# Performance work log

Hardware: AMD Instinct MI355X
Metric: run time of the kernel (lower is better)

Reference implementation:

```python
import jax, jax.numpy as jnp
import numpy as np

N = 10000      # cells (nodes)
F_IN = 512     # genes (features)
H = 40         # hidden_dim
DEG = 16       # avg kNN degree
EPS = 1e-5     # GraphNorm eps


def gcn(x, W, b, src, dst, coef):
    # PyG GCNConv: transform then symmetric-normalized aggregate (+bias)
    h = x @ W                                   # [N, out]
    msg = h[src] * coef[:, None]                # [E, out]
    out = jax.ops.segment_sum(msg, dst, num_segments=N)
    return out + b


def graph_norm(x, weight, bias, alpha):
    # PyG GraphNorm over a single graph: mean/var across nodes, learnable mean scale
    mean = jnp.mean(x, axis=0, keepdims=True)
    shifted = x - alpha * mean
    var = jnp.mean(shifted * shifted, axis=0, keepdims=True)
    return weight * shifted * jax.lax.rsqrt(var + EPS) + bias


def setup_inputs() -> dict:
    key = jax.random.key(0)
    ks = jax.random.split(key, 8)
    x = jax.random.uniform(ks[0], (N, F_IN), dtype=jnp.float32)
    E = N * DEG
    src = jax.random.randint(ks[1], (E,), 0, N)
    dst = jax.random.randint(ks[2], (E,), 0, N)
    loop = jnp.arange(N)
    src = jnp.concatenate([src, loop])          # add self-loops (GCNConv default)
    dst = jnp.concatenate([dst, loop])

    def glorot(k, shape):
        lim = np.sqrt(6.0 / (shape[0] + shape[1])).astype(np.float32)
        return jax.random.uniform(k, shape, jnp.float32, -lim, lim)

    W1 = glorot(ks[3], (F_IN, H)); b1 = jnp.zeros((H,), jnp.float32)
    gn_w = jnp.ones((H,), jnp.float32)
    gn_b = jnp.zeros((H,), jnp.float32)
    gn_a = jnp.ones((H,), jnp.float32)          # mean_scale alpha
    Wm = glorot(ks[4], (H, F_IN)); bm = jnp.zeros((F_IN,), jnp.float32)
    Wd = glorot(ks[5], (H, F_IN)); bd = jnp.zeros((F_IN,), jnp.float32)
    Wp = glorot(ks[6], (H, F_IN)); bp = jnp.zeros((F_IN,), jnp.float32)
    return {"x": x, "src": src, "dst": dst, "W1": W1, "b1": b1,
            "gn_w": gn_w, "gn_b": gn_b, "gn_a": gn_a,
            "Wm": Wm, "bm": bm, "Wd": Wd, "bd": bd, "Wp": Wp, "bp": bp}


def reference(x, src, dst, W1, b1, gn_w, gn_b, gn_a, Wm, bm, Wd, bd, Wp, bp):
    # symmetric GCN normalization (self-loops already in edge list, so deg >= 1)
    deg = jax.ops.segment_sum(jnp.ones_like(src, dtype=x.dtype), dst, num_segments=N)
    dis = jax.lax.rsqrt(deg)
    coef = dis[src] * dis[dst]                  # [E]

    hidden = jax.nn.relu(graph_norm(gcn(x, W1, b1, src, dst, coef), gn_w, gn_b, gn_a))
    # Dropout(0.3) is identity at inference
    _mean = jnp.clip(jnp.exp(gcn(hidden, Wm, bm, src, dst, coef)), 1e-5, 1e6)
    _disp = jnp.clip(jax.nn.softplus(gcn(hidden, Wd, bd, src, dst, coef)), 1e-4, 1e4)
    _pi = jax.nn.sigmoid(gcn(hidden, Wp, bp, src, dst, coef))
    return (_mean, _disp, _pi)
```

## Files before the change

### kernel.cpp

```cpp
#include <hip/hip_runtime.h>
#include <math.h>

#define NN 10000
#define FIN 512
#define HD 40
#define GEPS 1e-5f

#define ZI4 ((2 * NN + 2 * HD) / 4)
#define MM1_BLOCKS ((NN + 15) / 16)
#define ZERO_BLOCKS ((ZI4 + 255) / 256)

typedef _Float16 h4 __attribute__((ext_vector_type(4)));
typedef float f4 __attribute__((ext_vector_type(4)));

__global__ void k_hist(const int* __restrict__ dst, int* __restrict__ cnt, int E) {
    int e = blockIdx.x * blockDim.x + threadIdx.x;
    if (e < E) atomicAdd(&cnt[dst[e]], 1);
}

__global__ __launch_bounds__(1024) void k_scan(const int* __restrict__ cnt,
                                               int* __restrict__ rowstart,
                                               float* __restrict__ dis) {
    __shared__ int lds[1024];
    const int t = threadIdx.x;
    const int start = t * 10;
    const int end = min(start + 10, NN);
    int s = 0;
    for (int i = start; i < end; ++i) s += cnt[i];
    lds[t] = s;
    __syncthreads();
    for (int off = 1; off < 1024; off <<= 1) {
        int v = (t >= off) ? lds[t - off] : 0;
        __syncthreads();
        lds[t] += v;
        __syncthreads();
    }
    int run = lds[t] - s;
    for (int i = start; i < end; ++i) {
        int c = cnt[i];
        rowstart[i] = run;
        run += c;
        dis[i] = rsqrtf((float)c);
    }
    if (end == NN) rowstart[NN] = run;
}

__global__ void k_fill(const int* __restrict__ src, const int* __restrict__ dst,
                       const int* __restrict__ rowstart, int* __restrict__ cur,
                       const float* __restrict__ dis, int2* __restrict__ csr, int E) {
    int e = blockIdx.x * blockDim.x + threadIdx.x;
    if (e >= E) return;
    int s = src[e], d = dst[e];
    int pos = rowstart[d] + atomicAdd(&cur[d], 1);
    int2 v;
    v.x = s;
    v.y = __float_as_int(dis[s] * dis[d]);
    csr[pos] = v;
}

__global__ void k_cvtW(const float* __restrict__ Wm, const float* __restrict__ Wd,
                       const float* __restrict__ Wp, _Float16* __restrict__ Whf) {
    int idx = blockIdx.x * 256 + threadIdx.x;
    if (idx >= 3 * 32 * 3 * 64) return;
    int lane = idx & 63;
    int kk   = (idx >> 6) % 3;
    int ct   = ((idx >> 6) / 3) % 32;
    int z    = idx / (64 * 3 * 32);
    const float* W = (z == 0) ? Wm : (z == 1) ? Wd : Wp;
    int col = ct * 16 + (lane & 15);
    h4 v;
#pragma unroll
    for (int j = 0; j < 4; ++j) {
        int krow = kk * 16 + (lane >> 4) * 4 + j;
        v[j] = (krow < HD) ? (_Float16)W[(size_t)krow * FIN + col] : (_Float16)0.f;
    }
    *(h4*)(Whf + (size_t)idx * 4) = v;
}

__global__ __launch_bounds__(256) void k_mm1z(const float* __restrict__ x,
                                              const float* __restrict__ W1,
                                              float* __restrict__ h1,
                                              int4* __restrict__ zbuf) {
    if (blockIdx.x >= MM1_BLOCKS) {
        int i = (blockIdx.x - MM1_BLOCKS) * 256 + threadIdx.x;
        if (i < ZI4) zbuf[i] = make_int4(0, 0, 0, 0);
        return;
    }
    __shared__ float red[256 * 41];
    const int tid = threadIdx.x;
    const int r = tid & 15;
    const int kg = tid >> 4;
    const int row = blockIdx.x * 16 + r;
    const int rowc = min(row, NN - 1);
    const float4* xr = (const float4*)(x + (size_t)rowc * FIN + kg * 32);
    float acc[HD];
#pragma unroll
    for (int c = 0; c < HD; ++c) acc[c] = 0.f;
#pragma unroll 2
    for (int q = 0; q < 8; ++q) {
        float4 xv = xr[q];
        const float* wbase = W1 + (size_t)(kg * 32 + q * 4) * HD;
#pragma unroll
        for (int kk = 0; kk < 4; ++kk) {
            float xs = (kk == 0) ? xv.x : (kk == 1) ? xv.y : (kk == 2) ? xv.z : xv.w;
#pragma unroll
            for (int c4 = 0; c4 < 10; ++c4) {
                float4 wv = *(const float4*)(wbase + kk * HD + c4 * 4);
                acc[c4 * 4 + 0] = fmaf(xs, wv.x, acc[c4 * 4 + 0]);
                acc[c4 * 4 + 1] = fmaf(xs, wv.y, acc[c4 * 4 + 1]);
                acc[c4 * 4 + 2] = fmaf(xs, wv.z, acc[c4 * 4 + 2]);
                acc[c4 * 4 + 3] = fmaf(xs, wv.w, acc[c4 * 4 + 3]);
            }
        }
    }
#pragma unroll
    for (int c = 0; c < HD; ++c) red[tid * 41 + c] = acc[c];
    __syncthreads();
    if (tid < 160) {
        int rr = tid / 10, c4 = tid % 10;
        float o0 = 0.f, o1 = 0.f, o2 = 0.f, o3 = 0.f;
#pragma unroll
        for (int kg2 = 0; kg2 < 16; ++kg2) {
            const float* p = &red[(kg2 * 16 + rr) * 41 + c4 * 4];
            o0 += p[0]; o1 += p[1]; o2 += p[2]; o3 += p[3];
        }
        int orow = blockIdx.x * 16 + rr;
        if (orow < NN)
            *(float4*)&h1[(size_t)orow * HD + c4 * 4] = make_float4(o0, o1, o2, o3);
    }
}

template <bool NORM>
__global__ __launch_bounds__(256) void k_gather(const int* __restrict__ rowstart,
                                                const int2* __restrict__ csr,
                                                const float* __restrict__ hin,
                                                const float* __restrict__ stats,
                                                const float* __restrict__ b1,
                                                const float* __restrict__ gw,
                                                const float* __restrict__ gb,
                                                const float* __restrict__ ga,
                                                float* __restrict__ aggout_f,
                                                _Float16* __restrict__ aggout_h) {
    __shared__ float4 part[256];
    __shared__ float csc[2 * HD];
    const int t = threadIdx.x;
    if (NORM) {
        if (t < HD) {
            float m   = stats[t] * (1.0f / NN);
            float ex2 = stats[HD + t] * (1.0f / NN);
            float a   = ga[t];
            float var = ex2 - 2.0f * a * m * m + a * a * m * m;
            float sc  = gw[t] * rsqrtf(var + GEPS);
            csc[t]      = sc;
            csc[HD + t] = sc * (b1[t] - a * m) + gb[t];
        }
        __syncthreads();
    }
    const int slot = blockIdx.x * 128 + (t & 127);
    const int half = t >> 7;
    float4 acc = make_float4(0.f, 0.f, 0.f, 0.f);
    if (slot < NN * 10) {
        const int n = slot / 10, c4 = slot % 10;
        const int j0 = rowstart[n], j1 = rowstart[n + 1];
        const int mid = j0 + ((j1 - j0 + 1) >> 1);
        const int ja = half ? mid : j0;
        const int jb = half ? j1 : mid;
        float4 sc, sh;
        if (NORM) {
            sc = ((const float4*)csc)[c4];
            sh = ((const float4*)csc)[10 + c4];
        }
        for (int j = ja; j < jb; j += 4) {
            const int jm = jb - 1;
            int2 e0 = csr[j];
            int2 e1 = csr[min(j + 1, jm)];
            int2 e2 = csr[min(j + 2, jm)];
            int2 e3 = csr[min(j + 3, jm)];
            float4 v0 = *(const float4*)&hin[(size_t)e0.x * HD + c4 * 4];
            float4 v1 = *(const float4*)&hin[(size_t)e1.x * HD + c4 * 4];
            float4 v2 = *(const float4*)&hin[(size_t)e2.x * HD + c4 * 4];
            float4 v3 = *(const float4*)&hin[(size_t)e3.x * HD + c4 * 4];
            float c0 = __int_as_float(e0.y);
            float c1 = (j + 1 < jb) ? __int_as_float(e1.y) : 0.f;
            float c2 = (j + 2 < jb) ? __int_as_float(e2.y) : 0.f;
            float c3 = (j + 3 < jb) ? __int_as_float(e3.y) : 0.f;
            if (NORM) {
                v0.x = fmaxf(fmaf(sc.x, v0.x, sh.x), 0.f);
                v0.y = fmaxf(fmaf(sc.y, v0.y, sh.y), 0.f);
                v0.z = fmaxf(fmaf(sc.z, v0.z, sh.z), 0.f);
                v0.w = fmaxf(fmaf(sc.w, v0.w, sh.w), 0.f);
                v1.x = fmaxf(fmaf(sc.x, v1.x, sh.x), 0.f);
                v1.y = fmaxf(fmaf(sc.y, v1.y, sh.y), 0.f);
                v1.z = fmaxf(fmaf(sc.z, v1.z, sh.z), 0.f);
                v1.w = fmaxf(fmaf(sc.w, v1.w, sh.w), 0.f);
                v2.x = fmaxf(fmaf(sc.x, v2.x, sh.x), 0.f);
                v2.y = fmaxf(fmaf(sc.y, v2.y, sh.y), 0.f);
                v2.z = fmaxf(fmaf(sc.z, v2.z, sh.z), 0.f);
                v2.w = fmaxf(fmaf(sc.w, v2.w, sh.w), 0.f);
                v3.x = fmaxf(fmaf(sc.x, v3.x, sh.x), 0.f);
                v3.y = fmaxf(fmaf(sc.y, v3.y, sh.y), 0.f);
                v3.z = fmaxf(fmaf(sc.z, v3.z, sh.z), 0.f);
                v3.w = fmaxf(fmaf(sc.w, v3.w, sh.w), 0.f);
            }
            acc.x = fmaf(v0.x, c0, fmaf(v1.x, c1, fmaf(v2.x, c2, fmaf(v3.x, c3, acc.x))));
            acc.y = fmaf(v0.y, c0, fmaf(v1.y, c1, fmaf(v2.y, c2, fmaf(v3.y, c3, acc.y))));
            acc.z = fmaf(v0.z, c0, fmaf(v1.z, c1, fmaf(v2.z, c2, fmaf(v3.z, c3, acc.z))));
            acc.w = fmaf(v0.w, c0, fmaf(v1.w, c1, fmaf(v2.w, c2, fmaf(v3.w, c3, acc.w))));
        }
    }
    part[t] = acc;
    __syncthreads();
    if (half == 0 && slot < NN * 10) {
        const int n = slot / 10, c4 = slot % 10;
        float4 p2 = part[t + 128];
        acc.x += p2.x; acc.y += p2.y; acc.z += p2.z; acc.w += p2.w;
        if (NORM) {
            h4 hv = { (_Float16)acc.x, (_Float16)acc.y, (_Float16)acc.z, (_Float16)acc.w };
            *(h4*)(aggout_h + (size_t)n * 48 + c4 * 4) = hv;
            if (c4 == 0) {
                h4 zv = { (_Float16)0.f, (_Float16)0.f, (_Float16)0.f, (_Float16)0.f };
                *(h4*)(aggout_h + (size_t)n * 48 + 40) = zv;
                *(h4*)(aggout_h + (size_t)n * 48 + 44) = zv;
            }
        } else {
            ((float4*)aggout_f)[slot] = acc;
        }
    }
}

__global__ __launch_bounds__(256) void k_stats(const float* __restrict__ agg1,
                                               const float* __restrict__ b1,
                                               float* __restrict__ stats) {
    __shared__ float s0[HD], s1[HD];
    if (threadIdx.x < HD) { s0[threadIdx.x] = 0.f; s1[threadIdx.x] = 0.f; }
    __syncthreads();
    const int gid = blockIdx.x * 256 + threadIdx.x;
    const int c4 = gid % 10;
    float4 bv = ((const float4*)b1)[c4];
    float4 a0 = make_float4(0.f, 0.f, 0.f, 0.f);
    float4 a1 = a0;
    for (int i4 = gid; i4 < NN * 10; i4 += 80 * 256) {
        float4 v = ((const float4*)agg1)[i4];
        v.x += bv.x; v.y += bv.y; v.z += bv.z; v.w += bv.w;
        a0.x += v.x; a0.y += v.y; a0.z += v.z; a0.w += v.w;
        a1.x = fmaf(v.x, v.x, a1.x);
        a1.y = fmaf(v.y, v.y, a1.y);
        a1.z = fmaf(v.z, v.z, a1.z);
        a1.w = fmaf(v.w, v.w, a1.w);
    }
    atomicAdd(&s0[c4 * 4 + 0], a0.x); atomicAdd(&s0[c4 * 4 + 1], a0.y);
    atomicAdd(&s0[c4 * 4 + 2], a0.z); atomicAdd(&s0[c4 * 4 + 3], a0.w);
    atomicAdd(&s1[c4 * 4 + 0], a1.x); atomicAdd(&s1[c4 * 4 + 1], a1.y);
    atomicAdd(&s1[c4 * 4 + 2], a1.z); atomicAdd(&s1[c4 * 4 + 3], a1.w);
    __syncthreads();
    if (threadIdx.x < HD) {
        atomicAdd(&stats[threadIdx.x], s0[threadIdx.x]);
        atomicAdd(&stats[HD + threadIdx.x], s1[threadIdx.x]);
    }
}

__device__ __forceinline__ float activate_rt(float z, int act) {
    if (act == 0) {
        return fminf(fmaxf(__expf(z), 1e-5f), 1e6f);
    } else if (act == 1) {
        float sp = fmaxf(z, 0.0f) + __logf(1.0f + __expf(-fabsf(z)));
        return fminf(fmaxf(sp, 1e-4f), 1e4f);
    }
    return __fdividef(1.0f, 1.0f + __expf(-z));
}

__global__ __launch_bounds__(256) void k_heads3m(const _Float16* __restrict__ agghh,
                                                 const _Float16* __restrict__ Whf,
                                                 const float* __restrict__ bm,
                                                 const float* __restrict__ bd,
                                                 const float* __restrict__ bp,
                                                 float* __restrict__ out) {
    const int z = blockIdx.z;
    const float* bias = (z == 0) ? bm : (z == 1) ? bd : bp;
    float* o = out + (size_t)z * NN * FIN;

    const int lane = threadIdx.x & 63;
    const int wv   = threadIdx.x >> 6;
    const int rowbase = blockIdx.x * 16;
    const int r16  = lane & 15;
    const int kgrp = lane >> 4;

    const _Float16* arow = agghh + (size_t)(rowbase + r16) * 48 + kgrp * 4;
    h4 g0 = *(const h4*)(arow);
    h4 g1 = *(const h4*)(arow + 16);
    h4 g2 = *(const h4*)(arow + 32);

    const int grow = rowbase + r16;
    float* orow = o + (size_t)grow * FIN;

#pragma unroll
    for (int i = 0; i < 8; ++i) {
        const int ct = wv * 8 + i;
        const _Float16* wb = Whf + ((size_t)(z * 32 + ct) * 3) * 256 + lane * 4;
        h4 w0 = *(const h4*)(wb);
        h4 w1 = *(const h4*)(wb + 256);
        h4 w2 = *(const h4*)(wb + 512);
        f4 acc = {0.f, 0.f, 0.f, 0.f};
        acc = __builtin_amdgcn_mfma_f32_16x16x16f16(w0, g0, acc, 0, 0, 0);
        acc = __builtin_amdgcn_mfma_f32_16x16x16f16(w1, g1, acc, 0, 0, 0);
        acc = __builtin_amdgcn_mfma_f32_16x16x16f16(w2, g2, acc, 0, 0, 0);
        const int col0 = ct * 16 + kgrp * 4;
        float4 bv = *(const float4*)&bias[col0];
        float4 ov;
        ov.x = activate_rt(acc[0] + bv.x, z);
        ov.y = activate_rt(acc[1] + bv.y, z);
        ov.z = activate_rt(acc[2] + bv.z, z);
        ov.w = activate_rt(acc[3] + bv.w, z);
        *(float4*)(orow + col0) = ov;
    }
}

extern "C" void kernel_launch(void* const* d_in, const int* in_sizes, int n_in,
                              void* d_out, int out_size, void* d_ws, size_t ws_size,
                              hipStream_t stream) {
    const float* x   = (const float*)d_in[0];
    const int*   src = (const int*)d_in[1];
    const int*   dst = (const int*)d_in[2];
    const float* W1  = (const float*)d_in[3];
    const float* b1  = (const float*)d_in[4];
    const float* gnw = (const float*)d_in[5];
    const float* gnb = (const float*)d_in[6];
    const float* gna = (const float*)d_in[7];
    const float* Wm  = (const float*)d_in[8];
    const float* bm  = (const float*)d_in[9];
    const float* Wd  = (const float*)d_in[10];
    const float* bd  = (const float*)d_in[11];
    const float* Wp  = (const float*)d_in[12];
    const float* bp  = (const float*)d_in[13];
    const int E = in_sizes[1];

    float*     ws       = (float*)d_ws;
    float*     h1       = ws;
    float*     agg1     = h1 + (size_t)NN * HD;
    int*       cnt      = (int*)(agg1 + (size_t)NN * HD);
    int*       cur      = cnt + NN;
    float*     stats    = (float*)(cur + NN);
    float*     dis      = stats + 2 * HD;
    int*       rowstart = (int*)(dis + NN);
    int2*      csr      = (int2*)(rowstart + NN + 2);
    _Float16*  Whf      = (_Float16*)(csr + E);
    _Float16*  agghh    = (_Float16*)h1;
    float*     out      = (float*)d_out;

    k_cvtW<<<(3 * 32 * 3 * 64 + 255) / 256, 256, 0, stream>>>(Wm, Wd, Wp, Whf);
    k_mm1z<<<MM1_BLOCKS + ZERO_BLOCKS, 256, 0, stream>>>(x, W1, h1, (int4*)cnt);
    k_hist<<<(E + 255) / 256, 256, 0, stream>>>(dst, cnt, E);
    k_scan<<<1, 1024, 0, stream>>>(cnt, rowstart, dis);
    k_fill<<<(E + 255) / 256, 256, 0, stream>>>(src, dst, rowstart, cur, dis, csr, E);
    const int gblocks = (NN * 10 + 127) / 128;
    k_gather<false><<<gblocks, 256, 0, stream>>>(rowstart, csr, h1, nullptr,
                                                 nullptr, nullptr, nullptr, nullptr,
                                                 agg1, nullptr);
    k_stats<<<80, 256, 0, stream>>>(agg1, b1, stats);
    k_gather<true><<<gblocks, 256, 0, stream>>>(rowstart, csr, agg1, stats,
                                                b1, gnw, gnb, gna,
                                                nullptr, agghh);
    dim3 hgrid(MM1_BLOCKS, 1, 3);
    k_heads3m<<<hgrid, 256, 0, stream>>>(agghh, Whf, bm, bd, bp, out);
}
```

Before: 120.3 us.

## Fold weight conversion into mm1 launch, vectorize scan, unroll gather by eight

The fp16 weight-conversion kernel becomes extra blocks of the first matmul kernel, which removes one launch. The single-block scan now handles 16 counts per thread with int4 loads and float4/int4 stores instead of a scalar loop over 10. The CSR gather loop is unrolled to 8 edges per iteration so more independent loads are in flight, at the cost of more registers and more wasted clamped loads on short rows.

```diff
diff --git a/kernel.cpp b/kernel.cpp
--- a/kernel.cpp
+++ b/kernel.cpp
@@ -9,6 +9,7 @@
 #define ZI4 ((2 * NN + 2 * HD) / 4)
 #define MM1_BLOCKS ((NN + 15) / 16)
 #define ZERO_BLOCKS ((ZI4 + 255) / 256)
+#define CVT_BLOCKS ((3 * 32 * 3 * 64 + 255) / 256)
 
 typedef _Float16 h4 __attribute__((ext_vector_type(4)));
 typedef float f4 __attribute__((ext_vector_type(4)));
@@ -23,10 +24,16 @@
                                                float* __restrict__ dis) {
     __shared__ int lds[1024];
     const int t = threadIdx.x;
-    const int start = t * 10;
-    const int end = min(start + 10, NN);
+    const int start = t * 16;
+    int4 c[4];
     int s = 0;
-    for (int i = start; i < end; ++i) s += cnt[i];
+    if (start < NN) {
+#pragma unroll
+        for (int q = 0; q < 4; ++q) {
+            c[q] = *(const int4*)(cnt + start + q * 4);
+            s += c[q].x + c[q].y + c[q].z + c[q].w;
+        }
+    }
     lds[t] = s;
     __syncthreads();
     for (int off = 1; off < 1024; off <<= 1) {
@@ -35,14 +42,20 @@
         lds[t] += v;
         __syncthreads();
     }
-    int run = lds[t] - s;
-    for (int i = start; i < end; ++i) {
-        int c = cnt[i];
-        rowstart[i] = run;
-        run += c;
-        dis[i] = rsqrtf((float)c);
-    }
-    if (end == NN) rowstart[NN] = run;
+    if (start < NN) {
+        int run = lds[t] - s;
+#pragma unroll
+        for (int q = 0; q < 4; ++q) {
+            int4 rs; float4 dv;
+            rs.x = run; dv.x = rsqrtf((float)c[q].x); run += c[q].x;
+            rs.y = run; dv.y = rsqrtf((float)c[q].y); run += c[q].y;
+            rs.z = run; dv.z = rsqrtf((float)c[q].z); run += c[q].z;
+            rs.w = run; dv.w = rsqrtf((float)c[q].w); run += c[q].w;
+            *(int4*)(rowstart + start + q * 4) = rs;
+            *(float4*)(dis + start + q * 4) = dv;
+        }
+        if (start + 16 == NN) rowstart[NN] = run;
+    }
 }
 
 __global__ void k_fill(const int* __restrict__ src, const int* __restrict__ dst,
@@ -58,29 +71,33 @@
     csr[pos] = v;
 }
 
-__global__ void k_cvtW(const float* __restrict__ Wm, const float* __restrict__ Wd,
-                       const float* __restrict__ Wp, _Float16* __restrict__ Whf) {
-    int idx = blockIdx.x * 256 + threadIdx.x;
-    if (idx >= 3 * 32 * 3 * 64) return;
-    int lane = idx & 63;
-    int kk   = (idx >> 6) % 3;
-    int ct   = ((idx >> 6) / 3) % 32;
-    int z    = idx / (64 * 3 * 32);
-    const float* W = (z == 0) ? Wm : (z == 1) ? Wd : Wp;
-    int col = ct * 16 + (lane & 15);
-    h4 v;
-#pragma unroll
-    for (int j = 0; j < 4; ++j) {
-        int krow = kk * 16 + (lane >> 4) * 4 + j;
-        v[j] = (krow < HD) ? (_Float16)W[(size_t)krow * FIN + col] : (_Float16)0.f;
-    }
-    *(h4*)(Whf + (size_t)idx * 4) = v;
-}
-
 __global__ __launch_bounds__(256) void k_mm1z(const float* __restrict__ x,
                                               const float* __restrict__ W1,
                                               float* __restrict__ h1,
-                                              int4* __restrict__ zbuf) {
+                                              int4* __restrict__ zbuf,
+                                              const float* __restrict__ Wm,
+                                              const float* __restrict__ Wd,
+                                              const float* __restrict__ Wp,
+                                              _Float16* __restrict__ Whf) {
+    if (blockIdx.x >= MM1_BLOCKS + ZERO_BLOCKS) {
+        int idx = (blockIdx.x - MM1_BLOCKS - ZERO_BLOCKS) * 256 + threadIdx.x;
+        if (idx < 3 * 32 * 3 * 64) {
+            int lane = idx & 63;
+            int kk   = (idx >> 6) % 3;
+            int ct   = ((idx >> 6) / 3) % 32;
+            int z    = idx / (64 * 3 * 32);
+            const float* W = (z == 0) ? Wm : (z == 1) ? Wd : Wp;
+            int col = ct * 16 + (lane & 15);
+            h4 v;
+#pragma unroll
+            for (int j = 0; j < 4; ++j) {
+                int krow = kk * 16 + (lane >> 4) * 4 + j;
+                v[j] = (krow < HD) ? (_Float16)W[(size_t)krow * FIN + col] : (_Float16)0.f;
+            }
+            *(h4*)(Whf + (size_t)idx * 4) = v;
+        }
+        return;
+    }
     if (blockIdx.x >= MM1_BLOCKS) {
         int i = (blockIdx.x - MM1_BLOCKS) * 256 + threadIdx.x;
         if (i < ZI4) zbuf[i] = make_int4(0, 0, 0, 0);
@@ -170,42 +187,29 @@
             sc = ((const float4*)csc)[c4];
             sh = ((const float4*)csc)[10 + c4];
         }
-        for (int j = ja; j < jb; j += 4) {
+        for (int j = ja; j < jb; j += 8) {
             const int jm = jb - 1;
-            int2 e0 = csr[j];
-            int2 e1 = csr[min(j + 1, jm)];
-            int2 e2 = csr[min(j + 2, jm)];
-            int2 e3 = csr[min(j + 3, jm)];
-            float4 v0 = *(const float4*)&hin[(size_t)e0.x * HD + c4 * 4];
-            float4 v1 = *(const float4*)&hin[(size_t)e1.x * HD + c4 * 4];
-            float4 v2 = *(const float4*)&hin[(size_t)e2.x * HD + c4 * 4];
-            float4 v3 = *(const float4*)&hin[(size_t)e3.x * HD + c4 * 4];
-            float c0 = __int_as_float(e0.y);
-            float c1 = (j + 1 < jb) ? __int_as_float(e1.y) : 0.f;
-            float c2 = (j + 2 < jb) ? __int_as_float(e2.y) : 0.f;
-            float c3 = (j + 3 < jb) ? __int_as_float(e3.y) : 0.f;
-            if (NORM) {
-                v0.x = fmaxf(fmaf(sc.x, v0.x, sh.x), 0.f);
-                v0.y = fmaxf(fmaf(sc.y, v0.y, sh.y), 0.f);
-                v0.z = fmaxf(fmaf(sc.z, v0.z, sh.z), 0.f);
-                v0.w = fmaxf(fmaf(sc.w, v0.w, sh.w), 0.f);
-                v1.x = fmaxf(fmaf(sc.x, v1.x, sh.x), 0.f);
-                v1.y = fmaxf(fmaf(sc.y, v1.y, sh.y), 0.f);
-                v1.z = fmaxf(fmaf(sc.z, v1.z, sh.z), 0.f);
-                v1.w = fmaxf(fmaf(sc.w, v1.w, sh.w), 0.f);
-                v2.x = fmaxf(fmaf(sc.x, v2.x, sh.x), 0.f);
-                v2.y = fmaxf(fmaf(sc.y, v2.y, sh.y), 0.f);
-                v2.z = fmaxf(fmaf(sc.z, v2.z, sh.z), 0.f);
-                v2.w = fmaxf(fmaf(sc.w, v2.w, sh.w), 0.f);
-                v3.x = fmaxf(fmaf(sc.x, v3.x, sh.x), 0.f);
-                v3.y = fmaxf(fmaf(sc.y, v3.y, sh.y), 0.f);
-                v3.z = fmaxf(fmaf(sc.z, v3.z, sh.z), 0.f);
-                v3.w = fmaxf(fmaf(sc.w, v3.w, sh.w), 0.f);
+            int2 e[8];
+#pragma unroll
+            for (int q = 0; q < 8; ++q) e[q] = csr[min(j + q, jm)];
+            float4 v[8];
+#pragma unroll
+            for (int q = 0; q < 8; ++q)
+                v[q] = *(const float4*)&hin[(size_t)e[q].x * HD + c4 * 4];
+#pragma unroll
+            for (int q = 0; q < 8; ++q) {
+                float cf = (j + q < jb) ? __int_as_float(e[q].y) : 0.f;
+                if (NORM) {
+                    v[q].x = fmaxf(fmaf(sc.x, v[q].x, sh.x), 0.f);
+                    v[q].y = fmaxf(fmaf(sc.y, v[q].y, sh.y), 0.f);
+                    v[q].z = fmaxf(fmaf(sc.z, v[q].z, sh.z), 0.f);
+                    v[q].w = fmaxf(fmaf(sc.w, v[q].w, sh.w), 0.f);
+                }
+                acc.x = fmaf(v[q].x, cf, acc.x);
+                acc.y = fmaf(v[q].y, cf, acc.y);
+                acc.z = fmaf(v[q].z, cf, acc.z);
+                acc.w = fmaf(v[q].w, cf, acc.w);
             }
-            acc.x = fmaf(v0.x, c0, fmaf(v1.x, c1, fmaf(v2.x, c2, fmaf(v3.x, c3, acc.x))));
-            acc.y = fmaf(v0.y, c0, fmaf(v1.y, c1, fmaf(v2.y, c2, fmaf(v3.y, c3, acc.y))));
-            acc.z = fmaf(v0.z, c0, fmaf(v1.z, c1, fmaf(v2.z, c2, fmaf(v3.z, c3, acc.z))));
-            acc.w = fmaf(v0.w, c0, fmaf(v1.w, c1, fmaf(v2.w, c2, fmaf(v3.w, c3, acc.w))));
         }
     }
     part[t] = acc;
@@ -347,8 +351,8 @@
     _Float16*  agghh    = (_Float16*)h1;
     float*     out      = (float*)d_out;
 
-    k_cvtW<<<(3 * 32 * 3 * 64 + 255) / 256, 256, 0, stream>>>(Wm, Wd, Wp, Whf);
-    k_mm1z<<<MM1_BLOCKS + ZERO_BLOCKS, 256, 0, stream>>>(x, W1, h1, (int4*)cnt);
+    k_mm1z<<<MM1_BLOCKS + ZERO_BLOCKS + CVT_BLOCKS, 256, 0, stream>>>(
+        x, W1, h1, (int4*)cnt, Wm, Wd, Wp, Whf);
     k_hist<<<(E + 255) / 256, 256, 0, stream>>>(dst, cnt, E);
     k_scan<<<1, 1024, 0, stream>>>(cnt, rowstart, dis);
     k_fill<<<(E + 255) / 256, 256, 0, stream>>>(src, dst, rowstart, cur, dis, csr, E);
```

New measurement: 110.3 us. -8.3%, faster.
